# Optimization experiments

Measured on AMD Instinct MI355X. Metric: run time of the kernel, lower is better.

## Reference

```python
import jax, jax.numpy as jnp
import numpy as np

TEMPERATURE = 0.5  # init temperature; attn_drop=0.0 so dropout is identity


def setup_inputs() -> dict:
    key = jax.random.key(0)
    k1, k2, k3 = jax.random.split(key, 3)
    B, H, N, D = 4, 8, 2048, 64
    q = jax.random.normal(k1, (B, H, N, D), dtype=jnp.float32)
    k = jax.random.normal(k2, (B, H, N, D), dtype=jnp.float32)
    v = jax.random.normal(k3, (B, H, N, D), dtype=jnp.float32)
    scale = jnp.asarray(D ** -0.5, dtype=jnp.float32)
    return {"q": q, "k": k, "v": v, "scale": scale}


def reference(q, k, v, scale):
    # logits: [B,H,N,N]
    logits = jnp.einsum("bhqd,bhkd->bhqk", q, k) * scale
    # first softmax acts as a soft mask over keys
    soft_mask = jax.nn.softmax(logits / TEMPERATURE, axis=-1)
    # second softmax over masked logits (elementwise product, NOT matmul)
    attn = jax.nn.softmax(logits * soft_mask, axis=-1)
    # dropout with p=0.0 is identity
    out = jnp.einsum("bhqk,bhkd->bhqd", attn, v)
    return out
```

## Files before the change

### kernel.cpp

```cpp
#include <hip/hip_runtime.h>


typedef _Float16 f16;
typedef f16 f16x8 __attribute__((ext_vector_type(8)));
typedef f16 f16x4 __attribute__((ext_vector_type(4)));
typedef float f32x4 __attribute__((ext_vector_type(4)));

#define MFMA32(a, b, c) __builtin_amdgcn_mfma_f32_16x16x32_f16((a), (b), (c), 0, 0, 0)
#define MFMA16(a, b, c) __builtin_amdgcn_mfma_f32_16x16x16f16((a), (b), (c), 0, 0, 0)
#define EXP2(x) __builtin_amdgcn_exp2f(x)

#define N_CTX 2048
#define DH 64
#define KT 64
#define NKT (N_CTX / KT)
#define ROWS 128
#define QS 72

#define C2 2.885390081777927f

__device__ inline unsigned pk(float a, float b) {
    typedef __fp16 fp16x2_t __attribute__((ext_vector_type(2)));
    union { fp16x2_t v; unsigned u; } x;
    x.v = __builtin_amdgcn_cvt_pkrtz(a, b);
    return x.u;
}

__global__ __launch_bounds__(512, 4)
void stk_attn_mfma(const float* __restrict__ qg, const float* __restrict__ kg,
                   const float* __restrict__ vglob, const float* __restrict__ sg,
                   float* __restrict__ og) {
    __shared__ f16 Ks[2][KT * QS];
    __shared__ f16 Vt[2][DH * QS];

    const int tid  = threadIdx.x;
    const int wv   = tid >> 6;
    const int lane = tid & 63;
    const int l15  = lane & 15;
    const int q4   = lane >> 4;
    const int vp   = tid & 31;
    const int vgr  = tid >> 5;
    const int bh   = blockIdx.x & 31;
    const int q0   = (blockIdx.x >> 5) * ROWS;
    const float scale2 = sg[0] * C2;

    const float* qb = qg + (size_t)bh * N_CTX * DH;
    const float* kb = kg + (size_t)bh * N_CTX * DH;
    const float* vb = vglob + (size_t)bh * N_CTX * DH;
    float*       ob = og + (size_t)bh * N_CTX * DH;

    f16x8 aq[2];
    {
        const float* qrow = qb + (size_t)(q0 + wv * 16 + l15) * DH;
        #pragma unroll
        for (int kc = 0; kc < 2; ++kc) {
            float4 a0 = *(const float4*)&qrow[kc * 32 + q4 * 8];
            float4 a1 = *(const float4*)&qrow[kc * 32 + q4 * 8 + 4];
            union { f16x8 h; unsigned u[4]; } A;
            A.u[0] = pk(a0.x * scale2, a0.y * scale2);
            A.u[1] = pk(a0.z * scale2, a0.w * scale2);
            A.u[2] = pk(a1.x * scale2, a1.y * scale2);
            A.u[3] = pk(a1.z * scale2, a1.w * scale2);
            aq[kc] = A.h;
        }
    }

    f16* const ks_w  = &Ks[0][0];
    const f16* const ks_r = &Ks[0][l15 * QS + q4 * 8];
    f16* const vt_w  = &Vt[0][(vgr * 4) * QS + 2 * vp];
    const f16* const vt_r = &Vt[0][l15 * QS + q4 * 4];
    const int KSB = KT * QS;

    float s1 = 0.f;
    float4 kr[2];
    #pragma unroll
    for (int it = 0; it < 2; ++it) {
        int idx = it * 512 + tid;
        kr[it] = *(const float4*)&kb[((size_t)(idx >> 4)) * DH + (idx & 15) * 4];
    }
    #pragma unroll
    for (int it = 0; it < 2; ++it) {
        int idx = it * 512 + tid;
        *(uint2*)&ks_w[(idx >> 4) * QS + (idx & 15) * 4] =
            make_uint2(pk(kr[it].x, kr[it].y), pk(kr[it].z, kr[it].w));
    }
    #pragma unroll
    for (int it = 0; it < 2; ++it) {
        int idx = it * 512 + tid;
        kr[it] = *(const float4*)&kb[((size_t)KT + (idx >> 4)) * DH + (idx & 15) * 4];
    }
    __syncthreads();

    for (int kt = 0; kt < NKT; ++kt) {
        const int cur = (kt & 1) * KSB, nxt = KSB - cur;
        #pragma unroll
        for (int it = 0; it < 2; ++it) {
            int idx = it * 512 + tid;
            *(uint2*)&ks_w[nxt + (idx >> 4) * QS + (idx & 15) * 4] =
                make_uint2(pk(kr[it].x, kr[it].y), pk(kr[it].z, kr[it].w));
        }
        {
            int tn = (kt + 2 < NKT) ? kt + 2 : NKT - 1;
            #pragma unroll
            for (int it = 0; it < 2; ++it) {
                int idx = it * 512 + tid;
                kr[it] = *(const float4*)&kb[((size_t)tn * KT + (idx >> 4)) * DH + (idx & 15) * 4];
            }
        }
        __builtin_amdgcn_s_setprio(1);
        #pragma unroll
        for (int kgi = 0; kgi < 4; ++kgi) {
            f16x8 b0 = *(const f16x8*)&ks_r[cur + kgi * 16 * QS];
            f16x8 b1 = *(const f16x8*)&ks_r[cur + kgi * 16 * QS + 32];
            f32x4 acc = {0.f, 0.f, 0.f, 0.f};
            acc = MFMA32(b0, aq[0], acc);
            acc = MFMA32(b1, aq[1], acc);
            s1 += EXP2(acc[0]);
            s1 += EXP2(acc[1]);
            s1 += EXP2(acc[2]);
            s1 += EXP2(acc[3]);
        }
        __builtin_amdgcn_s_setprio(0);
        __syncthreads();
    }
    s1 += __shfl_xor(s1, 16, 64);
    s1 += __shfl_xor(s1, 32, 64);
    const float inv1 = 0.5f / s1;

    f32x4 O[4];
    #pragma unroll
    for (int dt = 0; dt < 4; ++dt) O[dt] = (f32x4){0.f, 0.f, 0.f, 0.f};
    f32x4 Oe = {0.f, 0.f, 0.f, 0.f};
    const f16x4 ones = {(f16)1.f, (f16)1.f, (f16)1.f, (f16)1.f};

    float4 vr0, vr1, vr2, vr3;
    #pragma unroll
    for (int it = 0; it < 2; ++it) {
        int idx = it * 512 + tid;
        kr[it] = *(const float4*)&kb[((size_t)(idx >> 4)) * DH + (idx & 15) * 4];
    }
    #pragma unroll
    for (int it = 0; it < 2; ++it) {
        int idx = it * 512 + tid;
        *(uint2*)&ks_w[(idx >> 4) * QS + (idx & 15) * 4] =
            make_uint2(pk(kr[it].x, kr[it].y), pk(kr[it].z, kr[it].w));
    }
    {
        const float* vs = vb + ((size_t)2 * vp) * DH + vgr * 4;
        float4 a0 = *(const float4*)(vs);
        float4 b0 = *(const float4*)(vs + DH);
        #pragma unroll
        for (int j = 0; j < 4; ++j)
            *(unsigned*)&vt_w[j * QS] = pk(((const float*)&a0)[j], ((const float*)&b0)[j]);
        const float* vs1 = vb + ((size_t)(KT + 2 * vp)) * DH + vgr * 4;
        vr0 = *(const float4*)(vs1);
        vr2 = *(const float4*)(vs1 + DH);
    }
    #pragma unroll
    for (int it = 0; it < 2; ++it) {
        int idx = it * 512 + tid;
        kr[it] = *(const float4*)&kb[((size_t)KT + (idx >> 4)) * DH + (idx & 15) * 4];
    }
    __syncthreads();

    for (int kt = 0; kt < NKT; ++kt) {
        const int cur = (kt & 1) * KSB, nxt = KSB - cur;
        #pragma unroll
        for (int it = 0; it < 2; ++it) {
            int idx = it * 512 + tid;
            *(uint2*)&ks_w[nxt + (idx >> 4) * QS + (idx & 15) * 4] =
                make_uint2(pk(kr[it].x, kr[it].y), pk(kr[it].z, kr[it].w));
        }
        #pragma unroll
        for (int j = 0; j < 4; ++j)
            *(unsigned*)&vt_w[nxt + j * QS] =
                pk(((const float*)&vr0)[j], ((const float*)&vr2)[j]);
        __builtin_amdgcn_s_setprio(1);
        f16x4 pfr[4];
        #pragma unroll
        for (int kgi = 0; kgi < 4; ++kgi) {
            f16x8 b0 = *(const f16x8*)&ks_r[cur + kgi * 16 * QS];
            f16x8 b1 = *(const f16x8*)&ks_r[cur + kgi * 16 * QS + 32];
            f32x4 acc = {0.f, 0.f, 0.f, 0.f};
            acc = MFMA32(b0, aq[0], acc);
            acc = MFMA32(b1, aq[1], acc);
            float e2r[4];
            #pragma unroll
            for (int r = 0; r < 4; ++r) {
                float a  = acc[r];
                float e1 = EXP2(a);
                e2r[r] = EXP2((a * e1) * inv1);
            }
            union { f16x4 h; unsigned u[2]; } P;
            P.u[0] = pk(e2r[0], e2r[1]);
            P.u[1] = pk(e2r[2], e2r[3]);
            pfr[kgi] = P.h;
            Oe = MFMA16(ones, pfr[kgi], Oe);
        }
        __builtin_amdgcn_s_setprio(0);
        {
            int tn = (kt + 2 < NKT) ? kt + 2 : NKT - 1;
            #pragma unroll
            for (int it = 0; it < 2; ++it) {
                int idx = it * 512 + tid;
                kr[it] = *(const float4*)&kb[((size_t)tn * KT + (idx >> 4)) * DH + (idx & 15) * 4];
            }
            const float* vs = vb + ((size_t)(tn * KT + 2 * vp)) * DH + vgr * 4;
            vr0 = *(const float4*)(vs);
            vr2 = *(const float4*)(vs + DH);
        }
        __builtin_amdgcn_s_setprio(1);
        #pragma unroll
        for (int kgi = 0; kgi < 4; ++kgi) {
            #pragma unroll
            for (int dt = 0; dt < 4; ++dt) {
                f16x4 av = *(const f16x4*)&vt_r[cur + dt * 16 * QS + kgi * 16];
                O[dt] = MFMA16(av, pfr[kgi], O[dt]);
            }
        }
        __builtin_amdgcn_s_setprio(0);
        __syncthreads();
    }

    const float invl2 = 1.0f / Oe[0];
    const size_t orow = (size_t)(q0 + wv * 16 + l15) * DH;
    #pragma unroll
    for (int dt = 0; dt < 4; ++dt) {
        float4 o;
        o.x = O[dt][0] * invl2;
        o.y = O[dt][1] * invl2;
        o.z = O[dt][2] * invl2;
        o.w = O[dt][3] * invl2;
        *(float4*)&ob[orow + dt * 16 + q4 * 4] = o;
    }
}

extern "C" void kernel_launch(void* const* d_in, const int* in_sizes, int n_in,
                              void* d_out, int out_size, void* d_ws, size_t ws_size,
                              hipStream_t stream) {
    const float* q = (const float*)d_in[0];
    const float* k = (const float*)d_in[1];
    const float* v = (const float*)d_in[2];
    const float* s = (const float*)d_in[3];
    float* out = (float*)d_out;
    dim3 grid(32 * 16);
    stk_attn_mfma<<<grid, 512, 0, stream>>>(q, k, v, s, out);
}
```

Before: 168.7 us.

## Permute V tile layout for 128-bit LDS reads and interleave QK with PV

Stores the transposed V tile in shared memory in a permuted column order so that each lane loads eight f16 values at once and splits them across two MFMA16 calls, halving the number of LDS reads for V. The second pass is restructured to compute the probability fragments two key groups at a time and consume them immediately in the PV MFMAs, and the next-tile global prefetch is now issued before this compute. Global and LDS offsets are hoisted into precomputed registers, and the first-pass exp sum is rebalanced into a tree. The change aims to cut LDS instruction count and shorten live ranges, at the cost of a more intricate index mapping that must match the MFMA operand layout exactly.

```diff
diff --git a/kernel.cpp b/kernel.cpp
--- a/kernel.cpp
+++ b/kernel.cpp
@@ -65,47 +65,46 @@
         }
     }
 
+    int kofs[2], gofs[2];
+    #pragma unroll
+    for (int it = 0; it < 2; ++it) {
+        int idx = it * 512 + tid;
+        gofs[it] = (idx >> 4) * DH + (idx & 15) * 4;
+        kofs[it] = (idx >> 4) * QS + (idx & 15) * 4;
+    }
+    const int c2p = ((vp >> 1) & 3) * 16 + (vp >> 3) * 4 + (vp & 1) * 2;
+
     f16* const ks_w  = &Ks[0][0];
     const f16* const ks_r = &Ks[0][l15 * QS + q4 * 8];
-    f16* const vt_w  = &Vt[0][(vgr * 4) * QS + 2 * vp];
-    const f16* const vt_r = &Vt[0][l15 * QS + q4 * 4];
+    f16* const vt_w  = &Vt[0][(vgr * 4) * QS + c2p];
+    const f16* const vt_r = &Vt[0][l15 * QS + q4 * 16];
     const int KSB = KT * QS;
 
     float s1 = 0.f;
     float4 kr[2];
     #pragma unroll
-    for (int it = 0; it < 2; ++it) {
-        int idx = it * 512 + tid;
-        kr[it] = *(const float4*)&kb[((size_t)(idx >> 4)) * DH + (idx & 15) * 4];
-    }
-    #pragma unroll
-    for (int it = 0; it < 2; ++it) {
-        int idx = it * 512 + tid;
-        *(uint2*)&ks_w[(idx >> 4) * QS + (idx & 15) * 4] =
+    for (int it = 0; it < 2; ++it)
+        kr[it] = *(const float4*)&kb[gofs[it]];
+    #pragma unroll
+    for (int it = 0; it < 2; ++it)
+        *(uint2*)&ks_w[kofs[it]] =
             make_uint2(pk(kr[it].x, kr[it].y), pk(kr[it].z, kr[it].w));
-    }
-    #pragma unroll
-    for (int it = 0; it < 2; ++it) {
-        int idx = it * 512 + tid;
-        kr[it] = *(const float4*)&kb[((size_t)KT + (idx >> 4)) * DH + (idx & 15) * 4];
-    }
+    #pragma unroll
+    for (int it = 0; it < 2; ++it)
+        kr[it] = *(const float4*)&kb[KT * DH + gofs[it]];
     __syncthreads();
 
     for (int kt = 0; kt < NKT; ++kt) {
         const int cur = (kt & 1) * KSB, nxt = KSB - cur;
         #pragma unroll
-        for (int it = 0; it < 2; ++it) {
-            int idx = it * 512 + tid;
-            *(uint2*)&ks_w[nxt + (idx >> 4) * QS + (idx & 15) * 4] =
+        for (int it = 0; it < 2; ++it)
+            *(uint2*)&ks_w[nxt + kofs[it]] =
                 make_uint2(pk(kr[it].x, kr[it].y), pk(kr[it].z, kr[it].w));
-        }
         {
             int tn = (kt + 2 < NKT) ? kt + 2 : NKT - 1;
             #pragma unroll
-            for (int it = 0; it < 2; ++it) {
-                int idx = it * 512 + tid;
-                kr[it] = *(const float4*)&kb[((size_t)tn * KT + (idx >> 4)) * DH + (idx & 15) * 4];
-            }
+            for (int it = 0; it < 2; ++it)
+                kr[it] = *(const float4*)&kb[(size_t)tn * KT * DH + gofs[it]];
         }
         __builtin_amdgcn_s_setprio(1);
         #pragma unroll
@@ -115,10 +114,7 @@
             f32x4 acc = {0.f, 0.f, 0.f, 0.f};
             acc = MFMA32(b0, aq[0], acc);
             acc = MFMA32(b1, aq[1], acc);
-            s1 += EXP2(acc[0]);
-            s1 += EXP2(acc[1]);
-            s1 += EXP2(acc[2]);
-            s1 += EXP2(acc[3]);
+            s1 += (EXP2(acc[0]) + EXP2(acc[1])) + (EXP2(acc[2]) + EXP2(acc[3]));
         }
         __builtin_amdgcn_s_setprio(0);
         __syncthreads();
@@ -133,18 +129,14 @@
     f32x4 Oe = {0.f, 0.f, 0.f, 0.f};
     const f16x4 ones = {(f16)1.f, (f16)1.f, (f16)1.f, (f16)1.f};
 
-    float4 vr0, vr1, vr2, vr3;
-    #pragma unroll
-    for (int it = 0; it < 2; ++it) {
-        int idx = it * 512 + tid;
-        kr[it] = *(const float4*)&kb[((size_t)(idx >> 4)) * DH + (idx & 15) * 4];
-    }
-    #pragma unroll
-    for (int it = 0; it < 2; ++it) {
-        int idx = it * 512 + tid;
-        *(uint2*)&ks_w[(idx >> 4) * QS + (idx & 15) * 4] =
+    float4 vr0, vr2;
+    #pragma unroll
+    for (int it = 0; it < 2; ++it)
+        kr[it] = *(const float4*)&kb[gofs[it]];
+    #pragma unroll
+    for (int it = 0; it < 2; ++it)
+        *(uint2*)&ks_w[kofs[it]] =
             make_uint2(pk(kr[it].x, kr[it].y), pk(kr[it].z, kr[it].w));
-    }
     {
         const float* vs = vb + ((size_t)2 * vp) * DH + vgr * 4;
         float4 a0 = *(const float4*)(vs);
@@ -157,65 +149,61 @@
         vr2 = *(const float4*)(vs1 + DH);
     }
     #pragma unroll
-    for (int it = 0; it < 2; ++it) {
-        int idx = it * 512 + tid;
-        kr[it] = *(const float4*)&kb[((size_t)KT + (idx >> 4)) * DH + (idx & 15) * 4];
-    }
+    for (int it = 0; it < 2; ++it)
+        kr[it] = *(const float4*)&kb[KT * DH + gofs[it]];
     __syncthreads();
 
     for (int kt = 0; kt < NKT; ++kt) {
         const int cur = (kt & 1) * KSB, nxt = KSB - cur;
         #pragma unroll
-        for (int it = 0; it < 2; ++it) {
-            int idx = it * 512 + tid;
-            *(uint2*)&ks_w[nxt + (idx >> 4) * QS + (idx & 15) * 4] =
+        for (int it = 0; it < 2; ++it)
+            *(uint2*)&ks_w[nxt + kofs[it]] =
                 make_uint2(pk(kr[it].x, kr[it].y), pk(kr[it].z, kr[it].w));
-        }
         #pragma unroll
         for (int j = 0; j < 4; ++j)
             *(unsigned*)&vt_w[nxt + j * QS] =
                 pk(((const float*)&vr0)[j], ((const float*)&vr2)[j]);
-        __builtin_amdgcn_s_setprio(1);
-        f16x4 pfr[4];
-        #pragma unroll
-        for (int kgi = 0; kgi < 4; ++kgi) {
-            f16x8 b0 = *(const f16x8*)&ks_r[cur + kgi * 16 * QS];
-            f16x8 b1 = *(const f16x8*)&ks_r[cur + kgi * 16 * QS + 32];
-            f32x4 acc = {0.f, 0.f, 0.f, 0.f};
-            acc = MFMA32(b0, aq[0], acc);
-            acc = MFMA32(b1, aq[1], acc);
-            float e2r[4];
-            #pragma unroll
-            for (int r = 0; r < 4; ++r) {
-                float a  = acc[r];
-                float e1 = EXP2(a);
-                e2r[r] = EXP2((a * e1) * inv1);
-            }
-            union { f16x4 h; unsigned u[2]; } P;
-            P.u[0] = pk(e2r[0], e2r[1]);
-            P.u[1] = pk(e2r[2], e2r[3]);
-            pfr[kgi] = P.h;
-            Oe = MFMA16(ones, pfr[kgi], Oe);
-        }
-        __builtin_amdgcn_s_setprio(0);
         {
             int tn = (kt + 2 < NKT) ? kt + 2 : NKT - 1;
             #pragma unroll
-            for (int it = 0; it < 2; ++it) {
-                int idx = it * 512 + tid;
-                kr[it] = *(const float4*)&kb[((size_t)tn * KT + (idx >> 4)) * DH + (idx & 15) * 4];
-            }
+            for (int it = 0; it < 2; ++it)
+                kr[it] = *(const float4*)&kb[(size_t)tn * KT * DH + gofs[it]];
             const float* vs = vb + ((size_t)(tn * KT + 2 * vp)) * DH + vgr * 4;
             vr0 = *(const float4*)(vs);
             vr2 = *(const float4*)(vs + DH);
         }
         __builtin_amdgcn_s_setprio(1);
         #pragma unroll
-        for (int kgi = 0; kgi < 4; ++kgi) {
+        for (int p = 0; p < 2; ++p) {
+            f16x4 pfr[2];
+            #pragma unroll
+            for (int h = 0; h < 2; ++h) {
+                const int kgi = p * 2 + h;
+                f16x8 b0 = *(const f16x8*)&ks_r[cur + kgi * 16 * QS];
+                f16x8 b1 = *(const f16x8*)&ks_r[cur + kgi * 16 * QS + 32];
+                f32x4 acc = {0.f, 0.f, 0.f, 0.f};
+                acc = MFMA32(b0, aq[0], acc);
+                acc = MFMA32(b1, aq[1], acc);
+                float e2r[4];
+                #pragma unroll
+                for (int r = 0; r < 4; ++r) {
+                    float a  = acc[r];
+                    float e1 = EXP2(a);
+                    e2r[r] = EXP2((a * e1) * inv1);
+                }
+                union { f16x4 hh; unsigned u[2]; } P;
+                P.u[0] = pk(e2r[0], e2r[1]);
+                P.u[1] = pk(e2r[2], e2r[3]);
+                pfr[h] = P.hh;
+                Oe = MFMA16(ones, pfr[h], Oe);
+            }
             #pragma unroll
             for (int dt = 0; dt < 4; ++dt) {
-                f16x4 av = *(const f16x4*)&vt_r[cur + dt * 16 * QS + kgi * 16];
-                O[dt] = MFMA16(av, pfr[kgi], O[dt]);
+                f16x8 av = *(const f16x8*)&vt_r[cur + dt * 16 * QS + p * 8];
+                f16x4 alo = __builtin_shufflevector(av, av, 0, 1, 2, 3);
+                f16x4 ahi = __builtin_shufflevector(av, av, 4, 5, 6, 7);
+                O[dt] = MFMA16(alo, pfr[0], O[dt]);
+                O[dt] = MFMA16(ahi, pfr[1], O[dt]);
             }
         }
         __builtin_amdgcn_s_setprio(0);
```

Result: no change. 166.1 us (-1.6%).
